# Optimization experiments

Measured on AMD Instinct MI355X. Metric: run time of the kernel, lower is better.

## Reference

```python
import jax, jax.numpy as jnp
import numpy as np

EPS = 1e-6      # zero-token detection eps
LN_EPS = 1e-5   # torch LayerNorm default
H = 8           # num_heads


def setup_inputs() -> dict:
    key = jax.random.key(0)
    ks = jax.random.split(key, 6)
    B, T, D = 4, 2048, 512
    embs = jax.random.normal(ks[0], (B, T, D), jnp.float32)
    labels = jax.random.uniform(ks[1], (B, T), jnp.float32)
    s = 1.0 / np.sqrt(D)
    ln_g = jnp.ones((D,), jnp.float32)
    ln_b = jnp.zeros((D,), jnp.float32)
    in_proj_w = jax.random.uniform(ks[2], (3 * D, D), jnp.float32, -s, s)
    in_proj_b = jnp.zeros((3 * D,), jnp.float32)
    out_w = jax.random.uniform(ks[3], (D, D), jnp.float32, -s, s)
    out_b = jnp.zeros((D,), jnp.float32)
    alpha = jnp.float32(1.0)
    beta = jnp.float32(0.0)
    return {"embs": embs, "labels": labels, "ln_g": ln_g, "ln_b": ln_b,
            "in_proj_w": in_proj_w, "in_proj_b": in_proj_b,
            "out_w": out_w, "out_b": out_b, "alpha": alpha, "beta": beta}


def reference(embs, labels, ln_g, ln_b, in_proj_w, in_proj_b, out_w, out_b, alpha, beta):
    B, T, D = embs.shape
    h, dh = H, D // H
    # pre-LayerNorm
    mu = embs.mean(-1, keepdims=True)
    var = ((embs - mu) ** 2).mean(-1, keepdims=True)
    x = (embs - mu) / jnp.sqrt(var + LN_EPS) * ln_g + ln_b
    # key padding mask from all-zero tokens (computed on normalized x, as in source)
    kpm = jnp.abs(x).sum(-1) <= EPS                      # [B,T] bool
    w = jnp.where(kpm, jnp.float32(0.0), labels)         # zero labels on masked tokens
    # fused qkv projection (nn.MultiheadAttention in_proj)
    qkv = x @ in_proj_w.T + in_proj_b                    # [B,T,3D]
    q, k, v = jnp.split(qkv, 3, axis=-1)
    def sp(a):
        return a.reshape(B, T, h, dh).transpose(0, 2, 1, 3)  # [B,h,T,dh]
    q, k, v = sp(q), sp(k), sp(v)
    scores = jnp.einsum('bhqd,bhkd->bhqk', q, k) / np.sqrt(dh)
    # additive label bias: alpha * labels (broadcast over heads & queries) + beta
    scores = scores + (alpha * w[:, None, None, :] + beta)
    # key padding mask -> -inf (use large negative for stability)
    scores = jnp.where(kpm[:, None, None, :], jnp.float32(-1e30), scores)
    a = jax.nn.softmax(scores, axis=-1)
    o = jnp.einsum('bhqk,bhkd->bhqd', a, v).transpose(0, 2, 1, 3).reshape(B, T, D)
    o = o @ out_w.T + out_b
    o = jnp.nan_to_num(o, nan=0.0, posinf=0.0, neginf=0.0)
    # masked mean pool over T
    m = (~kpm)[..., None].astype(o.dtype)                # [B,T,1]
    pooled = (o * m).sum(1) / jnp.maximum(m.sum(1), 1.0)  # [B,D]
    return pooled
```

## Files before the change

### kernel.cpp

```cpp
#include <hip/hip_runtime.h>
#include <math.h>

#define T 2048
#define D 512
#define NH 8
#define DH 64
#define NB 4
#define NTOK (NB * T)
#define LOG2E 1.44269504f
#define QSCALE (0.125f * LOG2E)

using bf16x8 = __attribute__((ext_vector_type(8))) short;
using f32x4  = __attribute__((ext_vector_type(4))) float;

static __device__ __forceinline__ unsigned short f2bf(float f) {
    union { float f; unsigned u; } v; v.f = f;
    unsigned r = v.u + 0x7fffu + ((v.u >> 16) & 1u);
    return (unsigned short)(r >> 16);
}
#if __has_builtin(__builtin_amdgcn_cvt_pk_bf16_f32)
static __device__ __forceinline__ unsigned pack_bf16_pair(float a, float b) {
    auto r = __builtin_amdgcn_cvt_pk_bf16_f32(a, b);
    union { decltype(r) v; unsigned u; } c; c.v = r;
    return c.u;
}
#else
static __device__ __forceinline__ unsigned pack_bf16_pair(float a, float b) {
    union { float f; unsigned u; } ua, ub; ua.f = a; ub.f = b;
    unsigned ra = ua.u + 0x7fffu + ((ua.u >> 16) & 1u);
    unsigned rb = ub.u + 0x7fffu + ((ub.u >> 16) & 1u);
    return __builtin_amdgcn_perm(rb, ra, 0x07060302);
}
#endif


__global__ __launch_bounds__(256) void ln_kernel(
    const float* __restrict__ embs, const float* __restrict__ labels,
    const float* __restrict__ g, const float* __restrict__ bb,
    const float* __restrict__ alpha_p, const float* __restrict__ beta_p,
    unsigned short* __restrict__ xfrag, float* __restrict__ wexp,
    float* __restrict__ kpmf)
{
    __shared__ __align__(16) unsigned short Xs[16][520];
    int tid = threadIdx.x, wave = tid >> 6, lane = tid & 63;
    int quad = lane >> 4, lm = lane & 15;
    int t16 = blockIdx.x;

    float4 g0 = *(const float4*)(g + lane * 8), g1 = *(const float4*)(g + lane * 8 + 4);
    float4 c0 = *(const float4*)(bb + lane * 8), c1 = *(const float4*)(bb + lane * 8 + 4);
    float gv[8] = {g0.x, g0.y, g0.z, g0.w, g1.x, g1.y, g1.z, g1.w};
    float cv[8] = {c0.x, c0.y, c0.z, c0.w, c1.x, c1.y, c1.z, c1.w};

    for (int tt = 0; tt < 4; ++tt) {
        int n = t16 * 16 + wave * 4 + tt;
        const float* e = embs + (size_t)n * D + lane * 8;
        float4 a4 = *(const float4*)e, b4 = *(const float4*)(e + 4);
        float v[8] = {a4.x, a4.y, a4.z, a4.w, b4.x, b4.y, b4.z, b4.w};

        float s = 0.f, ss = 0.f;
        #pragma unroll
        for (int j = 0; j < 8; ++j) { s += v[j]; ss += v[j] * v[j]; }
        #pragma unroll
        for (int o = 1; o <= 32; o <<= 1) {
            s += __shfl_xor(s, o, 64);
            ss += __shfl_xor(ss, o, 64);
        }
        float mu = s * (1.0f / D);
        float var = ss * (1.0f / D) - mu * mu;
        float rstd = rsqrtf(var + 1e-5f);

        float x[8], as = 0.f;
        #pragma unroll
        for (int j = 0; j < 8; ++j) {
            x[j] = (v[j] - mu) * rstd * gv[j] + cv[j];
            as += fabsf(x[j]);
        }
        uint4 pk;
        pk.x = pack_bf16_pair(x[0], x[1]);
        pk.y = pack_bf16_pair(x[2], x[3]);
        pk.z = pack_bf16_pair(x[4], x[5]);
        pk.w = pack_bf16_pair(x[6], x[7]);
        *(uint4*)&Xs[wave * 4 + tt][lane * 8] = pk;

        #pragma unroll
        for (int o = 1; o <= 32; o <<= 1) as += __shfl_xor(as, o, 64);
        if (lane == 0) {
            int kpm = (as <= 1e-6f);
            kpmf[n] = kpm ? 1.0f : 0.0f;
            wexp[n] = kpm ? 0.0f : __expf(alpha_p[0] * labels[n] + beta_p[0]);
        }
    }
    __syncthreads();
    #pragma unroll
    for (int i = 0; i < 4; ++i) {
        int kc = wave * 4 + i;
        bf16x8 fr = *(const bf16x8*)&Xs[lm][kc * 32 + quad * 8];
        *(bf16x8*)(xfrag + ((size_t)(t16 * 16 + kc) * 64 + lane) * 8) = fr;
    }
}

__global__ __launch_bounds__(256) void wconv_kernel(
    const float* __restrict__ w, unsigned short* __restrict__ wbfrag)
{
    __shared__ __align__(16) unsigned short Ws[16][520];
    int tid = threadIdx.x, wave = tid >> 6, lane = tid & 63;
    int quad = lane >> 4, lm = lane & 15;
    int j16 = blockIdx.x;

    for (int tt = 0; tt < 4; ++tt) {
        int j = j16 * 16 + wave * 4 + tt;
        const float* wp = w + (size_t)j * D + lane * 8;
        float4 a4 = *(const float4*)wp, b4 = *(const float4*)(wp + 4);
        uint4 pk;
        pk.x = pack_bf16_pair(a4.x, a4.y);
        pk.y = pack_bf16_pair(a4.z, a4.w);
        pk.z = pack_bf16_pair(b4.x, b4.y);
        pk.w = pack_bf16_pair(b4.z, b4.w);
        *(uint4*)&Ws[wave * 4 + tt][lane * 8] = pk;
    }
    __syncthreads();
    #pragma unroll
    for (int i = 0; i < 4; ++i) {
        int kc = wave * 4 + i;
        bf16x8 fr = *(const bf16x8*)&Ws[lm][kc * 32 + quad * 8];
        *(bf16x8*)(wbfrag + ((size_t)(j16 * 16 + kc) * 64 + lane) * 8) = fr;
    }
}

__global__ __launch_bounds__(256) void wfrag_fill(
    const float* __restrict__ wexp, unsigned short* __restrict__ vfrag)
{
    int idx = blockIdx.x * 256 + threadIdx.x;
    int lane = idx & 63, chunk = idx >> 6;
    int kk = chunk & 1, t64 = (chunk >> 1) & 31, bh = chunk >> 6;
    int lm = lane & 15, quad = lane >> 4;
    int b_ = bh >> 3;
    size_t base = (((size_t)chunk * 5 + 4) * 64 + lane) * 8;
    if (lm == 0) {
        int key0 = t64 * 64 + kk * 32 + quad * 8;
        const float* wp = wexp + b_ * T + key0;
        unsigned short vv[8];
        #pragma unroll
        for (int e = 0; e < 8; ++e) vv[e] = f2bf(wp[e]);
        *(uint4*)(vfrag + base) = *(uint4*)vv;
    } else {
        uint4 z = {0u, 0u, 0u, 0u};
        *(uint4*)(vfrag + base) = z;
    }
}

__global__ __launch_bounds__(256) void qkv_mfma(
    const unsigned short* __restrict__ xfrag, const unsigned short* __restrict__ wbfrag,
    const float* __restrict__ bias, const float* __restrict__ wexp,
    unsigned short* __restrict__ qfrag, unsigned short* __restrict__ kfrag,
    unsigned short* __restrict__ vfrag)
{
    __shared__ __align__(16) unsigned short Ls[4][64][72];
    int tid = threadIdx.x;
    int wave = tid >> 6, lane = tid & 63, quad = lane >> 4, lm = lane & 15;
    int wr = wave >> 1, wc = wave & 1;
    int m0 = blockIdx.x * 128 + wr * 64;
    int j0 = blockIdx.y * 128 + wc * 64;
    int mt16 = m0 >> 4, jt16 = j0 >> 4;

    f32x4 acc[4][4];
    #pragma unroll
    for (int a = 0; a < 4; ++a)
        #pragma unroll
        for (int b = 0; b < 4; ++b) acc[a][b] = (f32x4){0.f,0.f,0.f,0.f};

    for (int kc = 0; kc < 16; ++kc) {
        bf16x8 af[4], bf[4];
        #pragma unroll
        for (int mf = 0; mf < 4; ++mf)
            af[mf] = *(const bf16x8*)(xfrag + ((size_t)((mt16 + mf) * 16 + kc) * 64 + lane) * 8);
        #pragma unroll
        for (int nt = 0; nt < 4; ++nt)
            bf[nt] = *(const bf16x8*)(wbfrag + ((size_t)((jt16 + nt) * 16 + kc) * 64 + lane) * 8);
        #pragma unroll
        for (int mf = 0; mf < 4; ++mf)
            #pragma unroll
            for (int nt = 0; nt < 4; ++nt)
                acc[mf][nt] = __builtin_amdgcn_mfma_f32_16x16x32_bf16(af[mf], bf[nt], acc[mf][nt], 0, 0, 0);
    }

    int part = j0 >> 9;
    int h = (j0 & 511) >> 6;
    int b_ = m0 >> 11, tloc = m0 & (T - 1);
    int bh = b_ * NH + h;
    float bcol[4];
    #pragma unroll
    for (int nt = 0; nt < 4; ++nt) bcol[nt] = bias[j0 + nt * 16 + lm];

    if (part == 2) {
        float wv[4][4];
        #pragma unroll
        for (int mf = 0; mf < 4; ++mf)
            #pragma unroll
            for (int r = 0; r < 4; ++r)
                wv[mf][r] = wexp[b_ * T + tloc + mf * 16 + quad * 4 + r];
        #pragma unroll
        for (int mf = 0; mf < 4; ++mf)
            #pragma unroll
            for (int nt = 0; nt < 4; ++nt) {
                uint2 pw;
                pw.x = pack_bf16_pair((acc[mf][nt][0] + bcol[nt]) * wv[mf][0],
                                      (acc[mf][nt][1] + bcol[nt]) * wv[mf][1]);
                pw.y = pack_bf16_pair((acc[mf][nt][2] + bcol[nt]) * wv[mf][2],
                                      (acc[mf][nt][3] + bcol[nt]) * wv[mf][3]);
                *(uint2*)&Ls[wave][nt * 16 + lm][mf * 16 + quad * 4] = pw;
            }
        #pragma unroll
        for (int nt = 0; nt < 4; ++nt)
            #pragma unroll
            for (int kk = 0; kk < 2; ++kk) {
                bf16x8 fr = *(const bf16x8*)&Ls[wave][nt * 16 + lm][kk * 32 + quad * 8];
                size_t chunk = (((size_t)bh * 32 + (tloc >> 6)) * 2 + kk) * 5 + nt;
                *(bf16x8*)(vfrag + chunk * 512 + lane * 8) = fr;
            }
    } else {
        float scale = (part == 0) ? QSCALE : 1.0f;
        #pragma unroll
        for (int mf = 0; mf < 4; ++mf)
            #pragma unroll
            for (int nt = 0; nt < 4; ++nt)
                #pragma unroll
                for (int r = 0; r < 4; ++r)
                    Ls[wave][mf * 16 + quad * 4 + r][nt * 16 + lm] =
                        f2bf((acc[mf][nt][r] + bcol[nt]) * scale);
        if (part == 0) {
            #pragma unroll
            for (int mf = 0; mf < 4; ++mf)
                #pragma unroll
                for (int kk = 0; kk < 2; ++kk) {
                    bf16x8 fr = *(const bf16x8*)&Ls[wave][mf * 16 + lm][kk * 32 + quad * 8];
                    size_t chunk = ((size_t)bh * 128 + (tloc >> 4) + mf) * 2 + kk;
                    *(bf16x8*)(qfrag + chunk * 512 + lane * 8) = fr;
                }
        } else {
            #pragma unroll
            for (int nta = 0; nta < 4; ++nta)
                #pragma unroll
                for (int kk = 0; kk < 2; ++kk) {
                    bf16x8 fr = *(const bf16x8*)&Ls[wave][lm * 4 + nta][kk * 32 + quad * 8];
                    size_t chunk = (((size_t)bh * 32 + (tloc >> 6)) * 2 + kk) * 4 + nta;
                    *(bf16x8*)(kfrag + chunk * 512 + lane * 8) = fr;
                }
        }
    }
}

__global__ __launch_bounds__(256) void attn_mfma(
    const unsigned short* __restrict__ qfrag, const unsigned short* __restrict__ kfrag,
    const unsigned short* __restrict__ vfrag, const float* __restrict__ kpmf,
    float* __restrict__ S)
{
    __shared__ __align__(16) unsigned short Ps[128][72];
    int g = blockIdx.x;
    int bh = g & 31, q0 = (g >> 5) * 128;
    int tid = threadIdx.x, wave = tid >> 6, lane = tid & 63;
    int quad = lane >> 4, lm = lane & 15;
    int b_ = bh >> 3, h = bh & 7;

    bf16x8 qf[2][2];
    int t32 = (q0 >> 5) + wave;
    #pragma unroll
    for (int mf = 0; mf < 2; ++mf)
        #pragma unroll
        for (int kk = 0; kk < 2; ++kk)
            qf[mf][kk] = *(const bf16x8*)(qfrag +
                ((((size_t)(bh * 64 + t32) * 2 + mf) * 2 + kk) * 64 + lane) * 8);

    f32x4 accO[2][4], accL[2];
    #pragma unroll
    for (int mf = 0; mf < 2; ++mf) {
        #pragma unroll
        for (int nt = 0; nt < 4; ++nt) accO[mf][nt] = (f32x4){0.f,0.f,0.f,0.f};
        accL[mf] = (f32x4){0.f,0.f,0.f,0.f};
    }

    for (int t64 = 0; t64 < 32; ++t64) {
        bf16x8 kf[4][2], vf[5][2];
        #pragma unroll
        for (int kk = 0; kk < 2; ++kk)
            #pragma unroll
            for (int nt = 0; nt < 4; ++nt)
                kf[nt][kk] = *(const bf16x8*)(kfrag +
                    (((size_t)(bh * 32 + t64) * 2 + kk) * 4 + nt) * 512 + lane * 8);
        #pragma unroll
        for (int kk = 0; kk < 2; ++kk)
            #pragma unroll
            for (int nt = 0; nt < 5; ++nt)
                vf[nt][kk] = *(const bf16x8*)(vfrag +
                    (((size_t)(bh * 32 + t64) * 2 + kk) * 5 + nt) * 512 + lane * 8);

        f32x4 s[2][4];
        #pragma unroll
        for (int mf = 0; mf < 2; ++mf)
            #pragma unroll
            for (int nt = 0; nt < 4; ++nt) {
                f32x4 t0 = (f32x4){0.f,0.f,0.f,0.f};
                t0 = __builtin_amdgcn_mfma_f32_16x16x32_bf16(qf[mf][0], kf[nt][0], t0, 0, 0, 0);
                t0 = __builtin_amdgcn_mfma_f32_16x16x32_bf16(qf[mf][1], kf[nt][1], t0, 0, 0, 0);
                s[mf][nt] = t0;
            }

        #pragma unroll
        for (int mf = 0; mf < 2; ++mf) {
            int rowb = wave * 32 + mf * 16 + quad * 4;
            #pragma unroll
            for (int r = 0; r < 4; ++r) {
                float p0 = __builtin_amdgcn_exp2f(s[mf][0][r]);
                float p1 = __builtin_amdgcn_exp2f(s[mf][1][r]);
                float p2 = __builtin_amdgcn_exp2f(s[mf][2][r]);
                float p3 = __builtin_amdgcn_exp2f(s[mf][3][r]);
                uint2 pw;
                pw.x = pack_bf16_pair(p0, p1);
                pw.y = pack_bf16_pair(p2, p3);
                *(uint2*)&Ps[rowb + r][lm * 4] = pw;
            }
        }

        bf16x8 pf[2][2];
        #pragma unroll
        for (int mf = 0; mf < 2; ++mf)
            #pragma unroll
            for (int kk = 0; kk < 2; ++kk)
                pf[mf][kk] = *(const bf16x8*)&Ps[wave * 32 + mf * 16 + lm][kk * 32 + quad * 8];

        #pragma unroll
        for (int mf = 0; mf < 2; ++mf) {
            #pragma unroll
            for (int nt = 0; nt < 4; ++nt) {
                accO[mf][nt] = __builtin_amdgcn_mfma_f32_16x16x32_bf16(pf[mf][0], vf[nt][0], accO[mf][nt], 0, 0, 0);
                accO[mf][nt] = __builtin_amdgcn_mfma_f32_16x16x32_bf16(pf[mf][1], vf[nt][1], accO[mf][nt], 0, 0, 0);
            }
            accL[mf] = __builtin_amdgcn_mfma_f32_16x16x32_bf16(pf[mf][0], vf[4][0], accL[mf], 0, 0, 0);
            accL[mf] = __builtin_amdgcn_mfma_f32_16x16x32_bf16(pf[mf][1], vf[4][1], accL[mf], 0, 0, 0);
        }
    }

    float pooled[4] = {0.f, 0.f, 0.f, 0.f};
    #pragma unroll
    for (int mf = 0; mf < 2; ++mf)
        #pragma unroll
        for (int r = 0; r < 4; ++r) {
            int row = q0 + wave * 32 + mf * 16 + quad * 4 + r;
            float l = __shfl(accL[mf][r], lane & 48, 64);
            float w = (1.0f - kpmf[b_ * T + row]) / l;
            #pragma unroll
            for (int nt = 0; nt < 4; ++nt) pooled[nt] += accO[mf][nt][r] * w;
        }
    #pragma unroll
    for (int nt = 0; nt < 4; ++nt) {
        pooled[nt] += __shfl_xor(pooled[nt], 16, 64);
        pooled[nt] += __shfl_xor(pooled[nt], 32, 64);
    }
    if (quad == 0) {
        #pragma unroll
        for (int nt = 0; nt < 4; ++nt)
            atomicAdd(&S[b_ * D + h * DH + nt * 16 + lm], pooled[nt]);
    }
}

__global__ __launch_bounds__(256) void out_kernel(
    const float* __restrict__ S, const float* __restrict__ kpmf,
    const float* __restrict__ Wo, const float* __restrict__ bo,
    float* __restrict__ out)
{
    __shared__ float Sl[512];
    __shared__ float cs[4];
    __shared__ float pr[4][64];
    int b_ = blockIdx.x >> 3;
    int cg = blockIdx.x & 7;
    int tid = threadIdx.x;
    int col = tid & 63, kq = tid >> 6;
    Sl[tid] = S[b_ * D + tid];
    Sl[tid + 256] = S[b_ * D + tid + 256];
    const float* kp = kpmf + b_ * T;
    float c = 0.f;
    for (int t = tid; t < T; t += 256) c += kp[t];
    #pragma unroll
    for (int o = 32; o; o >>= 1) c += __shfl_xor(c, o, 64);
    if ((tid & 63) == 0) cs[tid >> 6] = c;
    __syncthreads();
    float masked = cs[0] + cs[1] + cs[2] + cs[3];
    float cnt = (float)T - masked;
    float inv = 1.0f / fmaxf(cnt, 1.0f);

    int d = cg * 64 + col;
    const float4* wr4 = (const float4*)(Wo + (size_t)d * D + kq * 128);
    float dot = 0.f;
    #pragma unroll 8
    for (int i = 0; i < 32; ++i) {
        float4 w4 = wr4[i];
        int kbase = kq * 128 + i * 4;
        dot += Sl[kbase + 0] * w4.x + Sl[kbase + 1] * w4.y +
               Sl[kbase + 2] * w4.z + Sl[kbase + 3] * w4.w;
    }
    pr[kq][col] = dot;
    __syncthreads();
    if (kq == 0) {
        float tot = pr[0][col] + pr[1][col] + pr[2][col] + pr[3][col];
        out[b_ * D + d] = (tot + bo[d] * cnt) * inv;
    }
}

extern "C" void kernel_launch(void* const* d_in, const int* in_sizes, int n_in,
                              void* d_out, int out_size, void* d_ws, size_t ws_size,
                              hipStream_t stream) {
    const float* embs   = (const float*)d_in[0];
    const float* labels = (const float*)d_in[1];
    const float* ln_g   = (const float*)d_in[2];
    const float* ln_b   = (const float*)d_in[3];
    const float* ipw    = (const float*)d_in[4];
    const float* ipb    = (const float*)d_in[5];
    const float* ow     = (const float*)d_in[6];
    const float* obb    = (const float*)d_in[7];
    const float* alpha  = (const float*)d_in[8];
    const float* beta   = (const float*)d_in[9];
    float* out = (float*)d_out;

    unsigned short* xfrag  = (unsigned short*)d_ws;
    unsigned short* wbfrag = xfrag + (size_t)NTOK * D;
    unsigned short* qfrag  = wbfrag + (size_t)3 * D * D;
    unsigned short* kfrag  = qfrag + (size_t)NTOK * D;
    unsigned short* vfrag  = kfrag + (size_t)NTOK * D;
    float* wexp = (float*)(vfrag + (size_t)32 * 32 * 2 * 5 * 512);
    float* kpmf = wexp + NTOK;
    float* S    = kpmf + NTOK;

    hipMemsetAsync(S, 0, (size_t)NB * D * sizeof(float), stream);
    ln_kernel<<<NTOK / 16, 256, 0, stream>>>(embs, labels, ln_g, ln_b, alpha, beta,
                                             xfrag, wexp, kpmf);
    wconv_kernel<<<(3 * D) / 16, 256, 0, stream>>>(ipw, wbfrag);
    wfrag_fill<<<512, 256, 0, stream>>>(wexp, vfrag);
    dim3 gq(NTOK / 128, (3 * D) / 128);
    qkv_mfma<<<gq, 256, 0, stream>>>(xfrag, wbfrag, ipb, wexp, qfrag, kfrag, vfrag);
    attn_mfma<<<32 * (T / 128), 256, 0, stream>>>(qfrag, kfrag, vfrag, kpmf, S);
    out_kernel<<<NB * 8, 256, 0, stream>>>(S, kpmf, ow, obb, out);
}
```

Before: 177.6 us.

## Apply label bias as exp2 offset in attention, drop ones-column row-sum trick

The label bias now goes into the score before exp2 as a log2-scaled additive term, with masked keys set to a huge negative value. Previously V was prescaled by exp(bias) and an extra fragment column computed the row sums. This removes the wfrag_fill kernel, the weight multiply in the QKV epilogue and the extra MFMAs for row sums, which are now summed in registers and reduced with shuffles. It also doubles the query tile to 256 rows per block with launch_bounds(256,1) and double-buffers the K and A/B fragment loads in both GEMM loops. In exchange the grid is smaller and register pressure is higher.

```diff
diff --git a/kernel.cpp b/kernel.cpp
--- a/kernel.cpp
+++ b/kernel.cpp
@@ -38,7 +38,7 @@
     const float* __restrict__ embs, const float* __restrict__ labels,
     const float* __restrict__ g, const float* __restrict__ bb,
     const float* __restrict__ alpha_p, const float* __restrict__ beta_p,
-    unsigned short* __restrict__ xfrag, float* __restrict__ wexp,
+    unsigned short* __restrict__ xfrag, float* __restrict__ wscaled,
     float* __restrict__ kpmf)
 {
     __shared__ __align__(16) unsigned short Xs[16][520];
@@ -87,7 +87,8 @@
         if (lane == 0) {
             int kpm = (as <= 1e-6f);
             kpmf[n] = kpm ? 1.0f : 0.0f;
-            wexp[n] = kpm ? 0.0f : __expf(alpha_p[0] * labels[n] + beta_p[0]);
+            wscaled[n] = kpm ? -3.0e38f
+                             : (alpha_p[0] * labels[n] + beta_p[0]) * LOG2E;
         }
     }
     __syncthreads();
@@ -127,33 +128,10 @@
     }
 }
 
-__global__ __launch_bounds__(256) void wfrag_fill(
-    const float* __restrict__ wexp, unsigned short* __restrict__ vfrag)
-{
-    int idx = blockIdx.x * 256 + threadIdx.x;
-    int lane = idx & 63, chunk = idx >> 6;
-    int kk = chunk & 1, t64 = (chunk >> 1) & 31, bh = chunk >> 6;
-    int lm = lane & 15, quad = lane >> 4;
-    int b_ = bh >> 3;
-    size_t base = (((size_t)chunk * 5 + 4) * 64 + lane) * 8;
-    if (lm == 0) {
-        int key0 = t64 * 64 + kk * 32 + quad * 8;
-        const float* wp = wexp + b_ * T + key0;
-        unsigned short vv[8];
-        #pragma unroll
-        for (int e = 0; e < 8; ++e) vv[e] = f2bf(wp[e]);
-        *(uint4*)(vfrag + base) = *(uint4*)vv;
-    } else {
-        uint4 z = {0u, 0u, 0u, 0u};
-        *(uint4*)(vfrag + base) = z;
-    }
-}
-
 __global__ __launch_bounds__(256) void qkv_mfma(
     const unsigned short* __restrict__ xfrag, const unsigned short* __restrict__ wbfrag,
-    const float* __restrict__ bias, const float* __restrict__ wexp,
-    unsigned short* __restrict__ qfrag, unsigned short* __restrict__ kfrag,
-    unsigned short* __restrict__ vfrag)
+    const float* __restrict__ bias, unsigned short* __restrict__ qfrag,
+    unsigned short* __restrict__ kfrag, unsigned short* __restrict__ vfrag)
 {
     __shared__ __align__(16) unsigned short Ls[4][64][72];
     int tid = threadIdx.x;
@@ -169,19 +147,29 @@
         #pragma unroll
         for (int b = 0; b < 4; ++b) acc[a][b] = (f32x4){0.f,0.f,0.f,0.f};
 
-    for (int kc = 0; kc < 16; ++kc) {
-        bf16x8 af[4], bf[4];
+    bf16x8 af0[4], bf0[4], af1[4], bf1[4];
+    auto load_ab = [&](int kc, bf16x8 (&af)[4], bf16x8 (&bf)[4]) {
         #pragma unroll
         for (int mf = 0; mf < 4; ++mf)
             af[mf] = *(const bf16x8*)(xfrag + ((size_t)((mt16 + mf) * 16 + kc) * 64 + lane) * 8);
         #pragma unroll
         for (int nt = 0; nt < 4; ++nt)
             bf[nt] = *(const bf16x8*)(wbfrag + ((size_t)((jt16 + nt) * 16 + kc) * 64 + lane) * 8);
+    };
+    auto do_mfma = [&](bf16x8 (&af)[4], bf16x8 (&bf)[4]) {
         #pragma unroll
         for (int mf = 0; mf < 4; ++mf)
             #pragma unroll
             for (int nt = 0; nt < 4; ++nt)
                 acc[mf][nt] = __builtin_amdgcn_mfma_f32_16x16x32_bf16(af[mf], bf[nt], acc[mf][nt], 0, 0, 0);
+    };
+
+    load_ab(0, af0, bf0);
+    for (int kc = 0; kc < 16; kc += 2) {
+        load_ab(kc + 1, af1, bf1);
+        do_mfma(af0, bf0);
+        load_ab((kc + 2) & 15, af0, bf0);
+        do_mfma(af1, bf1);
     }
 
     int part = j0 >> 9;
@@ -193,21 +181,15 @@
     for (int nt = 0; nt < 4; ++nt) bcol[nt] = bias[j0 + nt * 16 + lm];
 
     if (part == 2) {
-        float wv[4][4];
-        #pragma unroll
-        for (int mf = 0; mf < 4; ++mf)
-            #pragma unroll
-            for (int r = 0; r < 4; ++r)
-                wv[mf][r] = wexp[b_ * T + tloc + mf * 16 + quad * 4 + r];
         #pragma unroll
         for (int mf = 0; mf < 4; ++mf)
             #pragma unroll
             for (int nt = 0; nt < 4; ++nt) {
                 uint2 pw;
-                pw.x = pack_bf16_pair((acc[mf][nt][0] + bcol[nt]) * wv[mf][0],
-                                      (acc[mf][nt][1] + bcol[nt]) * wv[mf][1]);
-                pw.y = pack_bf16_pair((acc[mf][nt][2] + bcol[nt]) * wv[mf][2],
-                                      (acc[mf][nt][3] + bcol[nt]) * wv[mf][3]);
+                pw.x = pack_bf16_pair(acc[mf][nt][0] + bcol[nt],
+                                      acc[mf][nt][1] + bcol[nt]);
+                pw.y = pack_bf16_pair(acc[mf][nt][2] + bcol[nt],
+                                      acc[mf][nt][3] + bcol[nt]);
                 *(uint2*)&Ls[wave][nt * 16 + lm][mf * 16 + quad * 4] = pw;
             }
         #pragma unroll
@@ -215,7 +197,7 @@
             #pragma unroll
             for (int kk = 0; kk < 2; ++kk) {
                 bf16x8 fr = *(const bf16x8*)&Ls[wave][nt * 16 + lm][kk * 32 + quad * 8];
-                size_t chunk = (((size_t)bh * 32 + (tloc >> 6)) * 2 + kk) * 5 + nt;
+                size_t chunk = (((size_t)bh * 32 + (tloc >> 6)) * 2 + kk) * 4 + nt;
                 *(bf16x8*)(vfrag + chunk * 512 + lane * 8) = fr;
             }
     } else {
@@ -250,70 +232,80 @@
     }
 }
 
-__global__ __launch_bounds__(256) void attn_mfma(
+__global__ __launch_bounds__(256, 1) void attn_mfma(
     const unsigned short* __restrict__ qfrag, const unsigned short* __restrict__ kfrag,
-    const unsigned short* __restrict__ vfrag, const float* __restrict__ kpmf,
-    float* __restrict__ S)
+    const unsigned short* __restrict__ vfrag, const float* __restrict__ wscaled,
+    const float* __restrict__ kpmf, float* __restrict__ S)
 {
-    __shared__ __align__(16) unsigned short Ps[128][72];
+    __shared__ __align__(16) unsigned short Ps[256][72];
     int g = blockIdx.x;
-    int bh = g & 31, q0 = (g >> 5) * 128;
+    int bh = g & 31, q0 = (g >> 5) * 256;
     int tid = threadIdx.x, wave = tid >> 6, lane = tid & 63;
     int quad = lane >> 4, lm = lane & 15;
     int b_ = bh >> 3, h = bh & 7;
 
-    bf16x8 qf[2][2];
-    int t32 = (q0 >> 5) + wave;
-    #pragma unroll
-    for (int mf = 0; mf < 2; ++mf)
+    bf16x8 qf[4][2];
+    int t16b = (q0 >> 4) + wave * 4;
+    #pragma unroll
+    for (int mf = 0; mf < 4; ++mf)
         #pragma unroll
         for (int kk = 0; kk < 2; ++kk)
             qf[mf][kk] = *(const bf16x8*)(qfrag +
-                ((((size_t)(bh * 64 + t32) * 2 + mf) * 2 + kk) * 64 + lane) * 8);
-
-    f32x4 accO[2][4], accL[2];
-    #pragma unroll
-    for (int mf = 0; mf < 2; ++mf) {
-        #pragma unroll
-        for (int nt = 0; nt < 4; ++nt) accO[mf][nt] = (f32x4){0.f,0.f,0.f,0.f};
-        accL[mf] = (f32x4){0.f,0.f,0.f,0.f};
-    }
-
-    for (int t64 = 0; t64 < 32; ++t64) {
-        bf16x8 kf[4][2], vf[5][2];
+                (((size_t)(bh * 128 + t16b + mf) * 2 + kk) * 64 + lane) * 8);
+
+    f32x4 accO[4][4];
+    float l_part[4][4];
+    #pragma unroll
+    for (int mf = 0; mf < 4; ++mf)
+        #pragma unroll
+        for (int nt = 0; nt < 4; ++nt) {
+            accO[mf][nt] = (f32x4){0.f,0.f,0.f,0.f};
+            l_part[mf][nt] = 0.f;
+        }
+
+    const unsigned short* kbase = kfrag + (size_t)bh * 32 * 8 * 512;
+    const unsigned short* vbase = vfrag + (size_t)bh * 32 * 8 * 512;
+    const float* wsb = wscaled + b_ * T;
+
+    bf16x8 kf0[4][2], kf1[4][2];
+    float4 b40, b41;
+    auto load_k = [&](int t64, bf16x8 (&kf)[4][2], float4& b4) {
         #pragma unroll
         for (int kk = 0; kk < 2; ++kk)
             #pragma unroll
             for (int nt = 0; nt < 4; ++nt)
-                kf[nt][kk] = *(const bf16x8*)(kfrag +
-                    (((size_t)(bh * 32 + t64) * 2 + kk) * 4 + nt) * 512 + lane * 8);
+                kf[nt][kk] = *(const bf16x8*)(kbase +
+                    ((size_t)(t64 * 2 + kk) * 4 + nt) * 512 + lane * 8);
+        b4 = *(const float4*)(wsb + t64 * 64 + lm * 4);
+    };
+
+    auto process = [&](int t64, bf16x8 (&kf)[4][2], float4 b4) {
+        bf16x8 vf[4][2];
         #pragma unroll
         for (int kk = 0; kk < 2; ++kk)
             #pragma unroll
-            for (int nt = 0; nt < 5; ++nt)
-                vf[nt][kk] = *(const bf16x8*)(vfrag +
-                    (((size_t)(bh * 32 + t64) * 2 + kk) * 5 + nt) * 512 + lane * 8);
-
-        f32x4 s[2][4];
-        #pragma unroll
-        for (int mf = 0; mf < 2; ++mf)
+            for (int nt = 0; nt < 4; ++nt)
+                vf[nt][kk] = *(const bf16x8*)(vbase +
+                    ((size_t)(t64 * 2 + kk) * 4 + nt) * 512 + lane * 8);
+
+        #pragma unroll
+        for (int mf = 0; mf < 4; ++mf) {
+            f32x4 s[4];
             #pragma unroll
             for (int nt = 0; nt < 4; ++nt) {
                 f32x4 t0 = (f32x4){0.f,0.f,0.f,0.f};
                 t0 = __builtin_amdgcn_mfma_f32_16x16x32_bf16(qf[mf][0], kf[nt][0], t0, 0, 0, 0);
                 t0 = __builtin_amdgcn_mfma_f32_16x16x32_bf16(qf[mf][1], kf[nt][1], t0, 0, 0, 0);
-                s[mf][nt] = t0;
+                s[nt] = t0;
             }
-
-        #pragma unroll
-        for (int mf = 0; mf < 2; ++mf) {
-            int rowb = wave * 32 + mf * 16 + quad * 4;
+            int rowb = wave * 64 + mf * 16 + quad * 4;
             #pragma unroll
             for (int r = 0; r < 4; ++r) {
-                float p0 = __builtin_amdgcn_exp2f(s[mf][0][r]);
-                float p1 = __builtin_amdgcn_exp2f(s[mf][1][r]);
-                float p2 = __builtin_amdgcn_exp2f(s[mf][2][r]);
-                float p3 = __builtin_amdgcn_exp2f(s[mf][3][r]);
+                float p0 = __builtin_amdgcn_exp2f(s[0][r] + b4.x);
+                float p1 = __builtin_amdgcn_exp2f(s[1][r] + b4.y);
+                float p2 = __builtin_amdgcn_exp2f(s[2][r] + b4.z);
+                float p3 = __builtin_amdgcn_exp2f(s[3][r] + b4.w);
+                l_part[mf][r] += (p0 + p1) + (p2 + p3);
                 uint2 pw;
                 pw.x = pack_bf16_pair(p0, p1);
                 pw.y = pack_bf16_pair(p2, p3);
@@ -321,33 +313,47 @@
             }
         }
 
-        bf16x8 pf[2][2];
-        #pragma unroll
-        for (int mf = 0; mf < 2; ++mf)
+        bf16x8 pf[4][2];
+        #pragma unroll
+        for (int mf = 0; mf < 4; ++mf)
             #pragma unroll
             for (int kk = 0; kk < 2; ++kk)
-                pf[mf][kk] = *(const bf16x8*)&Ps[wave * 32 + mf * 16 + lm][kk * 32 + quad * 8];
-
-        #pragma unroll
-        for (int mf = 0; mf < 2; ++mf) {
+                pf[mf][kk] = *(const bf16x8*)&Ps[wave * 64 + mf * 16 + lm][kk * 32 + quad * 8];
+
+        #pragma unroll
+        for (int mf = 0; mf < 4; ++mf)
             #pragma unroll
             for (int nt = 0; nt < 4; ++nt) {
                 accO[mf][nt] = __builtin_amdgcn_mfma_f32_16x16x32_bf16(pf[mf][0], vf[nt][0], accO[mf][nt], 0, 0, 0);
                 accO[mf][nt] = __builtin_amdgcn_mfma_f32_16x16x32_bf16(pf[mf][1], vf[nt][1], accO[mf][nt], 0, 0, 0);
             }
-            accL[mf] = __builtin_amdgcn_mfma_f32_16x16x32_bf16(pf[mf][0], vf[4][0], accL[mf], 0, 0, 0);
-            accL[mf] = __builtin_amdgcn_mfma_f32_16x16x32_bf16(pf[mf][1], vf[4][1], accL[mf], 0, 0, 0);
-        }
-    }
+    };
+
+    load_k(0, kf0, b40);
+    for (int t64 = 0; t64 < 32; t64 += 2) {
+        load_k(t64 + 1, kf1, b41);
+        process(t64, kf0, b40);
+        load_k((t64 + 2) & 31, kf0, b40);
+        process(t64 + 1, kf1, b41);
+    }
+
+    #pragma unroll
+    for (int mf = 0; mf < 4; ++mf)
+        #pragma unroll
+        for (int r = 0; r < 4; ++r) {
+            float lv = l_part[mf][r];
+            #pragma unroll
+            for (int off = 1; off <= 8; off <<= 1) lv += __shfl_xor(lv, off, 64);
+            l_part[mf][r] = lv;
+        }
 
     float pooled[4] = {0.f, 0.f, 0.f, 0.f};
     #pragma unroll
-    for (int mf = 0; mf < 2; ++mf)
+    for (int mf = 0; mf < 4; ++mf)
         #pragma unroll
         for (int r = 0; r < 4; ++r) {
-            int row = q0 + wave * 32 + mf * 16 + quad * 4 + r;
-            float l = __shfl(accL[mf][r], lane & 48, 64);
-            float w = (1.0f - kpmf[b_ * T + row]) / l;
+            int row = q0 + wave * 64 + mf * 16 + quad * 4 + r;
+            float w = (1.0f - kpmf[b_ * T + row]) / l_part[mf][r];
             #pragma unroll
             for (int nt = 0; nt < 4; ++nt) pooled[nt] += accO[mf][nt][r] * w;
         }
@@ -426,17 +432,16 @@
     unsigned short* qfrag  = wbfrag + (size_t)3 * D * D;
     unsigned short* kfrag  = qfrag + (size_t)NTOK * D;
     unsigned short* vfrag  = kfrag + (size_t)NTOK * D;
-    float* wexp = (float*)(vfrag + (size_t)32 * 32 * 2 * 5 * 512);
-    float* kpmf = wexp + NTOK;
-    float* S    = kpmf + NTOK;
+    float* wscaled = (float*)(vfrag + (size_t)NTOK * D);
+    float* kpmf    = wscaled + NTOK;
+    float* S       = kpmf + NTOK;
 
     hipMemsetAsync(S, 0, (size_t)NB * D * sizeof(float), stream);
     ln_kernel<<<NTOK / 16, 256, 0, stream>>>(embs, labels, ln_g, ln_b, alpha, beta,
-                                             xfrag, wexp, kpmf);
+                                             xfrag, wscaled, kpmf);
     wconv_kernel<<<(3 * D) / 16, 256, 0, stream>>>(ipw, wbfrag);
-    wfrag_fill<<<512, 256, 0, stream>>>(wexp, vfrag);
     dim3 gq(NTOK / 128, (3 * D) / 128);
-    qkv_mfma<<<gq, 256, 0, stream>>>(xfrag, wbfrag, ipb, wexp, qfrag, kfrag, vfrag);
-    attn_mfma<<<32 * (T / 128), 256, 0, stream>>>(qfrag, kfrag, vfrag, kpmf, S);
+    qkv_mfma<<<gq, 256, 0, stream>>>(xfrag, wbfrag, ipb, qfrag, kfrag, vfrag);
+    attn_mfma<<<256, 256, 0, stream>>>(qfrag, kfrag, vfrag, wscaled, kpmf, S);
     out_kernel<<<NB * 8, 256, 0, stream>>>(S, kpmf, ow, obb, out);
 }
```

Result: no change. 174.8 us (-1.6%).
